# Performance work log

Measured on AMD Instinct MI355X. Metric: run time of the kernel, lower is better.

## Reference

```python
import jax, jax.numpy as jnp
import numpy as np

B, Cin, Cout, K, H, W = 16, 32, 32, 3, 256, 256
EMB = 256  # layer_pos_embedding_size == condition_size == 256


def setup_inputs() -> dict:
    key = jax.random.key(0)
    ks = jax.random.split(key, 7)
    return {
        "x": jax.random.normal(ks[0], (B, Cin, H, W), jnp.float32),
        "condition": jax.random.normal(ks[1], (B, EMB), jnp.float32),
        "layer_pos_embedding": jax.random.normal(ks[2], (B, EMB), jnp.float32),
        # base conv weight, stored [Cin, Cout, K, K] as in the torch module
        "weights": jax.random.normal(ks[3], (Cin, Cout, K, K), jnp.float32) * 0.05,
        "bias": jax.random.normal(ks[4], (Cout,), jnp.float32) * 0.05,
        # weightAdapt: Linear(2*EMB -> Cin); biasAdapt: Linear(2*EMB -> Cout)
        "wa_w": jax.random.normal(ks[5], (Cin, 2 * EMB), jnp.float32) * 0.04,
        "wa_b": jnp.zeros((Cin,), jnp.float32),
        "ba_w": jax.random.normal(ks[6], (Cout, 2 * EMB), jnp.float32) * 0.04,
        "ba_b": jnp.zeros((Cout,), jnp.float32),
    }


def reference(x, condition, layer_pos_embedding, weights, bias, wa_w, wa_b, ba_w, ba_b):
    # i = cat([condition, layer_pos_embedding])  -> [B, 2*EMB]
    i = jnp.concatenate([condition, layer_pos_embedding], axis=-1)
    wadapt = i @ wa_w.T + wa_b   # [B, Cin]  per-sample input-channel modulation
    badapt = i @ ba_w.T + ba_b   # [B, Cout] per-sample bias modulation
    # per-sample OIHW kernel: (weights [Cin,Cout,K,K] * wadapt[b,Cin,1,1,1]) rearranged
    kern = jnp.einsum('iokl,bi->boikl', weights, wadapt)  # [B, Cout, Cin, K, K]

    def conv1(xi, ki):
        # xi: [Cin,H,W], ki: [Cout,Cin,K,K] -> [Cout,H,W], padding='same', stride 1
        return jax.lax.conv_general_dilated(
            xi[None], ki, window_strides=(1, 1), padding='SAME',
            dimension_numbers=('NCHW', 'OIHW', 'NCHW'))[0]

    o = jax.vmap(conv1)(x, kern)  # [B, Cout, H, W] (== groups=batch grouped conv)
    # modulated bias add per (batch, out_channel)
    return o + (bias[None, :] * badapt)[:, :, None, None]
```

## Files before the change

### kernel.cpp

```cpp
#include <hip/hip_runtime.h>


#define B_    16
#define CIN   32
#define COUT  32
#define H_    256
#define W_    256
#define EMB2  512

#define XPX   66
#define PXS   32
#define ROWS_ (XPX*PXS)
#define NSLOT 8

using short8  = __attribute__((ext_vector_type(8))) short;
using float4v = __attribute__((ext_vector_type(4))) float;
using float4r = __attribute__((ext_vector_type(4))) float;

__device__ __forceinline__ unsigned short f2bf(float f) {
    unsigned u = __builtin_bit_cast(unsigned, f);
    u += 0x7FFFu + ((u >> 16) & 1u);
    return (unsigned short)(u >> 16);
}
__device__ __forceinline__ unsigned pk2(float a, float b) {
    return (unsigned)f2bf(a) | ((unsigned)f2bf(b) << 16);
}

__global__ __launch_bounds__(256) void adapt_kernel(
    const float* __restrict__ cond, const float* __restrict__ lpe,
    const float* __restrict__ wa_w, const float* __restrict__ wa_b,
    const float* __restrict__ ba_w, const float* __restrict__ ba_b,
    const float* __restrict__ bias, float* __restrict__ ws)
{
    __shared__ float iv[EMB2];
    __shared__ float partial[64][4];
    const int b = blockIdx.x;
    const int t = threadIdx.x;

    iv[t]       = cond[b*256 + t];
    iv[t + 256] = lpe[b*256 + t];
    __syncthreads();

    const int out  = t & 63;
    const int part = t >> 6;
    const float* row = (out < 32) ? (wa_w + out*EMB2) : (ba_w + (out-32)*EMB2);
    float s = 0.f;
    #pragma unroll 8
    for (int j = part*128; j < part*128 + 128; ++j) s += iv[j] * row[j];
    partial[out][part] = s;
    __syncthreads();

    if (t < 64) {
        float v = partial[t][0] + partial[t][1] + partial[t][2] + partial[t][3];
        if (t < 32) ws[b*32 + t] = v + wa_b[t];
        else {
            int o = t - 32;
            ws[512 + b*32 + o] = bias[o] * (v + ba_b[o]);
        }
    }
}

__global__ __launch_bounds__(256, 3) void conv_kernel(
    const float* __restrict__ x, const float* __restrict__ weights,
    const float* __restrict__ ws, float* __restrict__ out)
{
    __shared__ __align__(16) unsigned short xbuf[NSLOT * ROWS_];
    __shared__ __align__(16) unsigned short wbuf[9 * 2 * 64 * 8];

    const int tid    = threadIdx.x;
    const int lane   = tid & 63;
    const int w      = tid >> 6;
    const int ln15   = lane & 15;
    const int kg     = lane >> 4;
    const int xstrip = blockIdx.x * 64;
    const int ystrip = blockIdx.y * 32;
    const int b      = blockIdx.z;

    for (int idx = tid; idx < CIN*COUT*9; idx += 256) {
        int i   = idx / 288;
        int rem = idx - i*288;
        int o   = rem / 9;
        int tap = rem - o*9;
        float v = weights[idx] * ws[b*32 + i];
        wbuf[((tap*2 + (o>>4))*64 + ((i>>3)*16 + (o&15)))*8 + (i&7)] = f2bf(v);
    }

    auto ld_main = [&](int gy, int g, int q, float4r (&L)[8]) {
        if ((unsigned)gy < 256u) {
            const float* src = x + (((size_t)(b*CIN + g*8) << 16) + (gy << 8)
                                    + (xstrip + 4*q));
            #pragma unroll
            for (int j = 0; j < 8; ++j)
                L[j] = *(const float4r*)&src[(size_t)j << 16];
        } else {
            #pragma unroll
            for (int j = 0; j < 8; ++j) L[j] = float4r{0.f, 0.f, 0.f, 0.f};
        }
    };
    auto wr_main = [&](int r, int g, int q, const float4r (&L)[8]) {
        unsigned slot = (unsigned)(r + 1) & 7;
        #pragma unroll
        for (int n = 0; n < 4; ++n) {
            int k = (n + q) & 3;
            int p = 4*q + k + 1;
            uint4 pk;
            pk.x = pk2(L[0][k], L[1][k]);
            pk.y = pk2(L[2][k], L[3][k]);
            pk.z = pk2(L[4][k], L[5][k]);
            pk.w = pk2(L[6][k], L[7][k]);
            *(uint4*)&xbuf[slot*ROWS_ + p*PXS + ((g ^ ((p >> 1) & 3)) * 8)] = pk;
        }
    };
    auto load8 = [&](int g, int yy, int xx, float (&f)[8]) {
        if (((unsigned)yy < 256u) & ((unsigned)xx < 256u)) {
            const float* src = x + (((size_t)(b*CIN + g*8) << 16) + (yy << 8) + xx);
            #pragma unroll
            for (int j = 0; j < 8; ++j) f[j] = src[(size_t)j << 16];
        } else {
            #pragma unroll
            for (int j = 0; j < 8; ++j) f[j] = 0.f;
        }
    };
    auto packwrite = [&](int r, int p, int g, const float (&f)[8]) {
        unsigned slot = (unsigned)(r + 1) & 7;
        unsigned dst  = slot*ROWS_ + p*PXS + ((g ^ ((p >> 1) & 3)) * 8);
        uint4 pk;
        pk.x = pk2(f[0], f[1]); pk.y = pk2(f[2], f[3]);
        pk.z = pk2(f[4], f[5]); pk.w = pk2(f[6], f[7]);
        *(uint4*)&xbuf[dst] = pk;
    };

    #pragma unroll
    for (int k2 = 0; k2 < 2; ++k2) {
        int ci = tid + k2*256;
        if (ci < 384) {
            int q = ci & 15, g = (ci >> 4) & 3, rr = ci >> 6;
            float4r L[8];
            ld_main(ystrip + rr - 1, g, q, L);
            wr_main(rr - 1, g, q, L);
        }
    }
    if (tid < 48) {
        int s = tid & 1, g = (tid >> 1) & 3, rr = tid >> 3;
        int p = s ? 65 : 0;
        float f[8];
        load8(g, ystrip + rr - 1, xstrip + p - 1, f);
        packwrite(rr - 1, p, g, f);
    }

    float bm[2][4];
    #pragma unroll
    for (int ot = 0; ot < 2; ++ot)
        #pragma unroll
        for (int r = 0; r < 4; ++r)
            bm[ot][r] = ws[512 + b*32 + ot*16 + kg*4 + r];

    float4r PM[8];
    float   PH[8];
    auto pf_issue = [&](int r0) {
        int q = tid & 15, g = (tid >> 4) & 3, rr = tid >> 6;
        ld_main(ystrip + r0 + rr, g, q, PM);
        if (tid < 32) {
            int s = tid & 1, hg = (tid >> 1) & 3, hr = tid >> 3;
            int p = s ? 65 : 0;
            load8(hg, ystrip + r0 + hr, xstrip + p - 1, PH);
        }
    };
    auto pf_write = [&](int r0) {
        int q = tid & 15, g = (tid >> 4) & 3, rr = tid >> 6;
        wr_main(r0 + rr, g, q, PM);
        if (tid < 32) {
            int s = tid & 1, hg = (tid >> 1) & 3, hr = tid >> 3;
            int p = s ? 65 : 0;
            packwrite(r0 + hr, p, hg, PH);
        }
    };

    pf_issue(5);

    asm volatile("s_waitcnt lgkmcnt(0)" ::: "memory");
    __builtin_amdgcn_s_barrier();
    asm volatile("" ::: "memory");

    for (int t = 0; t < 8; ++t) {
        const int orow = 4*t + w;
        const int gy   = ystrip + orow;

        float4v acc[4][2];
        #pragma unroll
        for (int c = 0; c < 4; ++c) {
            acc[c][0] = float4v{0.f, 0.f, 0.f, 0.f};
            acc[c][1] = float4v{0.f, 0.f, 0.f, 0.f};
        }

        #pragma unroll
        for (int dy = 0; dy < 3; ++dy) {
            const int rowbase = ((orow + dy) & 7) * ROWS_;
            #pragma unroll
            for (int dx = 0; dx < 3; ++dx) {
                const int tap = dy*3 + dx;
                short8 a0 = *(const short8*)&wbuf[((tap*2 + 0)*64 + lane)*8];
                short8 a1 = *(const short8*)&wbuf[((tap*2 + 1)*64 + lane)*8];
                #pragma unroll
                for (int c = 0; c < 4; ++c) {
                    int p = c*16 + dx + ln15;
                    int a = rowbase + p*PXS + ((kg ^ ((p >> 1) & 3)) * 8);
                    short8 xf = *(const short8*)&xbuf[a];
                    acc[c][0] = __builtin_amdgcn_mfma_f32_16x16x32_bf16(
                                    a0, xf, acc[c][0], 0, 0, 0);
                    acc[c][1] = __builtin_amdgcn_mfma_f32_16x16x32_bf16(
                                    a1, xf, acc[c][1], 0, 0, 0);
                }
            }
        }

        asm volatile("s_waitcnt lgkmcnt(0)" ::: "memory");
        __builtin_amdgcn_s_barrier();
        asm volatile("" ::: "memory");

        if (t < 7) {
            pf_write(4*t + 5);
            if (t < 6) pf_issue(4*t + 9);
        }

        asm volatile("" ::: "memory");

        #pragma unroll
        for (int c = 0; c < 4; ++c) {
            const int xcol = xstrip + c*16 + ln15;
            #pragma unroll
            for (int ot = 0; ot < 2; ++ot) {
                const int obase = ot*16 + kg*4;
                #pragma unroll
                for (int r = 0; r < 4; ++r) {
                    out[((size_t)(b*COUT + obase + r)*256 + gy)*256 + xcol] =
                        acc[c][ot][r] + bm[ot][r];
                }
            }
        }

        if (t < 7) {
            asm volatile("s_waitcnt lgkmcnt(0)" ::: "memory");
            __builtin_amdgcn_s_barrier();
            asm volatile("" ::: "memory");
        }
    }
}

extern "C" void kernel_launch(void* const* d_in, const int* in_sizes, int n_in,
                              void* d_out, int out_size, void* d_ws, size_t ws_size,
                              hipStream_t stream) {
    const float* x       = (const float*)d_in[0];
    const float* cond    = (const float*)d_in[1];
    const float* lpe     = (const float*)d_in[2];
    const float* weights = (const float*)d_in[3];
    const float* bias    = (const float*)d_in[4];
    const float* wa_w    = (const float*)d_in[5];
    const float* wa_b    = (const float*)d_in[6];
    const float* ba_w    = (const float*)d_in[7];
    const float* ba_b    = (const float*)d_in[8];
    float* outp = (float*)d_out;
    float* ws   = (float*)d_ws;

    adapt_kernel<<<dim3(B_), dim3(256), 0, stream>>>(
        cond, lpe, wa_w, wa_b, ba_w, ba_b, bias, ws);

    conv_kernel<<<dim3(W_/64, H_/32, B_), dim3(256), 0, stream>>>(
        x, weights, ws, outp);
}
```

Baseline: 285.6 us.

## Reshape conv tile to 128x16 with six-slot row ring buffer

Changes each block's output tile from 64 columns by 32 rows to 128 columns by 16 rows. Each wave now computes eight 16-pixel column chunks per output row, so every weight fragment loaded from LDS is reused twice as many times. The LDS row ring shrinks from 8 to 6 slots (indexed with modulo), prefetch registers are doubled, and launch bounds drop to 2 blocks per CU. The cost is more vertical halo rows reloaded per block, higher register pressure and lower occupancy.

```diff
diff --git a/kernel.cpp b/kernel.cpp
--- a/kernel.cpp
+++ b/kernel.cpp
@@ -8,10 +8,11 @@
 #define W_    256
 #define EMB2  512
 
-#define XPX   66
+#define TW    128
+#define XPX   130
 #define PXS   32
 #define ROWS_ (XPX*PXS)
-#define NSLOT 8
+#define NSLOT 6
 
 using short8  = __attribute__((ext_vector_type(8))) short;
 using float4v = __attribute__((ext_vector_type(4))) float;
@@ -60,7 +61,7 @@
     }
 }
 
-__global__ __launch_bounds__(256, 3) void conv_kernel(
+__global__ __launch_bounds__(256, 2) void conv_kernel(
     const float* __restrict__ x, const float* __restrict__ weights,
     const float* __restrict__ ws, float* __restrict__ out)
 {
@@ -72,8 +73,8 @@
     const int w      = tid >> 6;
     const int ln15   = lane & 15;
     const int kg     = lane >> 4;
-    const int xstrip = blockIdx.x * 64;
-    const int ystrip = blockIdx.y * 32;
+    const int xstrip = blockIdx.x * TW;
+    const int ystrip = blockIdx.y * 16;
     const int b      = blockIdx.z;
 
     for (int idx = tid; idx < CIN*COUT*9; idx += 256) {
@@ -98,7 +99,7 @@
         }
     };
     auto wr_main = [&](int r, int g, int q, const float4r (&L)[8]) {
-        unsigned slot = (unsigned)(r + 1) & 7;
+        unsigned slot = (unsigned)(r + 1) % NSLOT;
         #pragma unroll
         for (int n = 0; n < 4; ++n) {
             int k = (n + q) & 3;
@@ -122,7 +123,7 @@
         }
     };
     auto packwrite = [&](int r, int p, int g, const float (&f)[8]) {
-        unsigned slot = (unsigned)(r + 1) & 7;
+        unsigned slot = (unsigned)(r + 1) % NSLOT;
         unsigned dst  = slot*ROWS_ + p*PXS + ((g ^ ((p >> 1) & 3)) * 8);
         uint4 pk;
         pk.x = pk2(f[0], f[1]); pk.y = pk2(f[2], f[3]);
@@ -131,18 +132,16 @@
     };
 
     #pragma unroll
-    for (int k2 = 0; k2 < 2; ++k2) {
+    for (int k2 = 0; k2 < 3; ++k2) {
         int ci = tid + k2*256;
-        if (ci < 384) {
-            int q = ci & 15, g = (ci >> 4) & 3, rr = ci >> 6;
-            float4r L[8];
-            ld_main(ystrip + rr - 1, g, q, L);
-            wr_main(rr - 1, g, q, L);
-        }
+        int q = ci & 31, g = (ci >> 5) & 3, rr = ci >> 7;
+        float4r L[8];
+        ld_main(ystrip + rr - 1, g, q, L);
+        wr_main(rr - 1, g, q, L);
     }
     if (tid < 48) {
         int s = tid & 1, g = (tid >> 1) & 3, rr = tid >> 3;
-        int p = s ? 65 : 0;
+        int p = s ? (TW + 1) : 0;
         float f[8];
         load8(g, ystrip + rr - 1, xstrip + p - 1, f);
         packwrite(rr - 1, p, g, f);
@@ -155,23 +154,39 @@
         for (int r = 0; r < 4; ++r)
             bm[ot][r] = ws[512 + b*32 + ot*16 + kg*4 + r];
 
-    float4r PM[8];
+    float4r PMa[8], PMb[8];
     float   PH[8];
     auto pf_issue = [&](int r0) {
-        int q = tid & 15, g = (tid >> 4) & 3, rr = tid >> 6;
-        ld_main(ystrip + r0 + rr, g, q, PM);
+        {
+            int ci = tid;
+            int q = ci & 31, g = (ci >> 5) & 3, rr = ci >> 7;
+            ld_main(ystrip + r0 + rr, g, q, PMa);
+        }
+        {
+            int ci = tid + 256;
+            int q = ci & 31, g = (ci >> 5) & 3, rr = ci >> 7;
+            ld_main(ystrip + r0 + rr, g, q, PMb);
+        }
         if (tid < 32) {
             int s = tid & 1, hg = (tid >> 1) & 3, hr = tid >> 3;
-            int p = s ? 65 : 0;
+            int p = s ? (TW + 1) : 0;
             load8(hg, ystrip + r0 + hr, xstrip + p - 1, PH);
         }
     };
     auto pf_write = [&](int r0) {
-        int q = tid & 15, g = (tid >> 4) & 3, rr = tid >> 6;
-        wr_main(r0 + rr, g, q, PM);
+        {
+            int ci = tid;
+            int q = ci & 31, g = (ci >> 5) & 3, rr = ci >> 7;
+            wr_main(r0 + rr, g, q, PMa);
+        }
+        {
+            int ci = tid + 256;
+            int q = ci & 31, g = (ci >> 5) & 3, rr = ci >> 7;
+            wr_main(r0 + rr, g, q, PMb);
+        }
         if (tid < 32) {
             int s = tid & 1, hg = (tid >> 1) & 3, hr = tid >> 3;
-            int p = s ? 65 : 0;
+            int p = s ? (TW + 1) : 0;
             packwrite(r0 + hr, p, hg, PH);
         }
     };
@@ -182,27 +197,27 @@
     __builtin_amdgcn_s_barrier();
     asm volatile("" ::: "memory");
 
-    for (int t = 0; t < 8; ++t) {
+    for (int t = 0; t < 4; ++t) {
         const int orow = 4*t + w;
         const int gy   = ystrip + orow;
 
-        float4v acc[4][2];
-        #pragma unroll
-        for (int c = 0; c < 4; ++c) {
+        float4v acc[8][2];
+        #pragma unroll
+        for (int c = 0; c < 8; ++c) {
             acc[c][0] = float4v{0.f, 0.f, 0.f, 0.f};
             acc[c][1] = float4v{0.f, 0.f, 0.f, 0.f};
         }
 
         #pragma unroll
         for (int dy = 0; dy < 3; ++dy) {
-            const int rowbase = ((orow + dy) & 7) * ROWS_;
+            const int rowbase = (int)((unsigned)(orow + dy) % NSLOT) * ROWS_;
             #pragma unroll
             for (int dx = 0; dx < 3; ++dx) {
                 const int tap = dy*3 + dx;
                 short8 a0 = *(const short8*)&wbuf[((tap*2 + 0)*64 + lane)*8];
                 short8 a1 = *(const short8*)&wbuf[((tap*2 + 1)*64 + lane)*8];
                 #pragma unroll
-                for (int c = 0; c < 4; ++c) {
+                for (int c = 0; c < 8; ++c) {
                     int p = c*16 + dx + ln15;
                     int a = rowbase + p*PXS + ((kg ^ ((p >> 1) & 3)) * 8);
                     short8 xf = *(const short8*)&xbuf[a];
@@ -218,15 +233,15 @@
         __builtin_amdgcn_s_barrier();
         asm volatile("" ::: "memory");
 
-        if (t < 7) {
+        if (t < 3) {
             pf_write(4*t + 5);
-            if (t < 6) pf_issue(4*t + 9);
+            if (t < 2) pf_issue(4*t + 9);
         }
 
         asm volatile("" ::: "memory");
 
         #pragma unroll
-        for (int c = 0; c < 4; ++c) {
+        for (int c = 0; c < 8; ++c) {
             const int xcol = xstrip + c*16 + ln15;
             #pragma unroll
             for (int ot = 0; ot < 2; ++ot) {
@@ -239,7 +254,7 @@
             }
         }
 
-        if (t < 7) {
+        if (t < 3) {
             asm volatile("s_waitcnt lgkmcnt(0)" ::: "memory");
             __builtin_amdgcn_s_barrier();
             asm volatile("" ::: "memory");
@@ -265,6 +280,6 @@
     adapt_kernel<<<dim3(B_), dim3(256), 0, stream>>>(
         cond, lpe, wa_w, wa_b, ba_w, ba_b, bias, ws);
 
-    conv_kernel<<<dim3(W_/64, H_/32, B_), dim3(256), 0, stream>>>(
+    conv_kernel<<<dim3(W_/TW, H_/16, B_), dim3(256), 0, stream>>>(
         x, weights, ws, outp);
 }
```

New measurement: 273.0 us. 1.05x faster.
